# Kernel optimization log

Measured on AMD Instinct MI355X. Metric: run time of the kernel, lower is better.

## Reference

```python
import jax, jax.numpy as jnp
import numpy as np


def _squash(t):
    # squash along axis=2 (the atoms axis of [B, D, A, 1, 1])
    norm = jnp.linalg.norm(t, axis=2, keepdims=True)
    n2 = norm * norm
    return t / norm * (n2 / (1.0 + n2))


def setup_inputs() -> dict:
    key = jax.random.key(0)
    k1, k2 = jax.random.split(key)
    B, I, Ain, D, A = 32, 2048, 16, 32, 16
    x = jax.random.normal(k1, (B, I, Ain, 1, 1), jnp.float32)
    weights = 0.1 * jax.random.normal(k2, (I, Ain, D * A, 1, 1), jnp.float32)
    bias = jnp.full((D, A, 1, 1), 0.1, jnp.float32)  # nn.init.constant_(0.1)
    return {"x": x, "weights": weights, "bias": bias, "num_routing": 3}


def reference(x, weights, bias, num_routing):
    B, I, Ain = x.shape[:3]
    D, A = bias.shape[:2]
    # Vote computation (standard voting): sum over input_atoms.
    # Torch does expand+mul+sum; einsum is the same math without the 4.8GB intermediate.
    votes = jnp.einsum('bia,iao->bio', x[:, :, :, 0, 0],
                       weights[:, :, :, 0, 0]).reshape(B, I, D, A, 1, 1)
    votes_sg = jax.lax.stop_gradient(votes)  # votes_trans_stopped in torch
    logits = jnp.zeros((B, I, D, 1, 1), x.dtype)
    activation = None
    for i in range(num_routing):
        route = jax.nn.softmax(logits, axis=2)  # [B, I, D, 1, 1], softmax over D
        v = votes if i == num_routing - 1 else votes_sg
        # route broadcast over atoms axis; sum over input capsules I
        preact = jnp.sum(route[:, :, :, None] * v, axis=1) + bias  # [B, D, A, 1, 1]
        activation = _squash(preact)
        if i < num_routing - 1:
            # agreement update uses non-stopped votes (as in torch)
            logits = logits + jnp.sum(votes * activation[:, None], axis=3)  # [B, I, D, 1, 1]
    return activation
```

## Files before the change

### kernel.cpp

```cpp
#include <hip/hip_runtime.h>


#define B_  32
#define I_  2048
#define K_  16
#define O_  512
#define NG_ 512
#define IC_ 4

typedef const __attribute__((address_space(1))) uint32_t* gp_t;
typedef __attribute__((address_space(3))) uint32_t* lp_t;

template<int PASS>
__global__ __launch_bounds__(512, 4)
void sweep_kernel(const float* __restrict__ x, const float* __restrict__ W,
                  const float* __restrict__ act0_g, const float* __restrict__ act1_g,
                  float* __restrict__ partial)
{
    const int tid  = threadIdx.x;
    const int lane = tid & 63;
    const int wave = tid >> 6;
    const int ig   = blockIdx.x;
    const int obase = lane * 8;

    const int wv    = __builtin_amdgcn_readfirstlane(wave);
    const int bbase = wv * 4;

    __shared__ float sW[K_ * O_];

    float facc[4][8];
    #pragma unroll
    for (int bb = 0; bb < 4; ++bb)
        #pragma unroll
        for (int j = 0; j < 8; ++j) facc[bb][j] = 0.f;

    float as[4][8];
    if (PASS >= 1) {
        #pragma unroll
        for (int bb = 0; bb < 4; ++bb) {
            const float4* p0 = (const float4*)(act0_g + (bbase + bb) * O_ + obase);
            float4 f0 = p0[0], f1 = p0[1];
            as[bb][0]=f0.x; as[bb][1]=f0.y; as[bb][2]=f0.z; as[bb][3]=f0.w;
            as[bb][4]=f1.x; as[bb][5]=f1.y; as[bb][6]=f1.z; as[bb][7]=f1.w;
            if (PASS == 2) {
                const float4* p1 = (const float4*)(act1_g + (bbase + bb) * O_ + obase);
                float4 g0 = p1[0], g1 = p1[1];
                as[bb][0]+=g0.x; as[bb][1]+=g0.y; as[bb][2]+=g0.z; as[bb][3]+=g0.w;
                as[bb][4]+=g1.x; as[bb][5]+=g1.y; as[bb][6]+=g1.z; as[bb][7]+=g1.w;
            }
        }
    }

    for (int ii = 0; ii < IC_; ++ii) {
        const int i = ig * IC_ + ii;
        __syncthreads();
        {
            const float* gsrc = W + (size_t)i * (K_ * O_);
            #pragma unroll
            for (int q = 0; q < 4; ++q) {
                const int fb = (wave * 4 + q) * 64;
                __builtin_amdgcn_global_load_lds(
                    (gp_t)(gsrc + 4 * (fb + lane)),
                    (lp_t)(&sW[4 * fb]), 16, 0, 0);
            }
        }
        float xs[4][16];
        #pragma unroll
        for (int bb = 0; bb < 4; ++bb) {
            const float4* xp = (const float4*)(x + ((size_t)(bbase + bb) * I_ + i) * K_);
            #pragma unroll
            for (int q = 0; q < 4; ++q) {
                float4 v = xp[q];
                xs[bb][4*q+0]=v.x; xs[bb][4*q+1]=v.y; xs[bb][4*q+2]=v.z; xs[bb][4*q+3]=v.w;
            }
        }
        __syncthreads();

        float V[4][8];
        #pragma unroll
        for (int bb = 0; bb < 4; ++bb)
            #pragma unroll
            for (int j = 0; j < 8; ++j) V[bb][j] = 0.f;
        #pragma unroll
        for (int k = 0; k < K_; ++k) {
            const float4 w0 = *(const float4*)&sW[k * O_ + obase];
            const float4 w1 = *(const float4*)&sW[k * O_ + obase + 4];
            const float w[8] = {w0.x, w0.y, w0.z, w0.w, w1.x, w1.y, w1.z, w1.w};
            #pragma unroll
            for (int bb = 0; bb < 4; ++bb) {
                const float xb = xs[bb][k];
                #pragma unroll
                for (int j = 0; j < 8; ++j) V[bb][j] = fmaf(xb, w[j], V[bb][j]);
            }
        }

        #pragma unroll
        for (int bb = 0; bb < 4; ++bb) {
            if (PASS == 0) {
                #pragma unroll
                for (int j = 0; j < 8; ++j) facc[bb][j] += V[bb][j];
            } else {
                float lg = 0.f;
                #pragma unroll
                for (int j = 0; j < 8; ++j) lg = fmaf(V[bb][j], as[bb][j], lg);
                lg += __shfl_xor(lg, 1);
                const float e = __expf(lg);
                float s = e;
                s += __shfl_xor(s, 2);
                s += __shfl_xor(s, 4);
                s += __shfl_xor(s, 8);
                s += __shfl_xor(s, 16);
                s += __shfl_xor(s, 32);
                const float r = e * __builtin_amdgcn_rcpf(s);
                #pragma unroll
                for (int j = 0; j < 8; ++j)
                    facc[bb][j] = fmaf(r, V[bb][j], facc[bb][j]);
            }
        }
    }

    #pragma unroll
    for (int bb = 0; bb < 4; ++bb) {
        const int b = bbase + bb;
        float4* dst = (float4*)(partial + ((size_t)ig * B_ + b) * O_ + obase);
        dst[0] = make_float4(facc[bb][0], facc[bb][1], facc[bb][2], facc[bb][3]);
        dst[1] = make_float4(facc[bb][4], facc[bb][5], facc[bb][6], facc[bb][7]);
    }
}

__global__ __launch_bounds__(256)
void reduce_squash(const float* __restrict__ partial, const float* __restrict__ bias,
                   float scale, float* __restrict__ out)
{
    const int t     = threadIdx.x;
    const int quad  = t & 15;
    const int slice = t >> 4;
    const int gbase = blockIdx.x * 64;
    const float4* src = (const float4*)partial + (gbase >> 2) + quad;

    float4 acc = make_float4(0.f, 0.f, 0.f, 0.f);
    #pragma unroll 8
    for (int w = slice * 32; w < slice * 32 + 32; ++w) {
        float4 v = src[(size_t)w * (B_ * O_ / 4)];
        acc.x += v.x; acc.y += v.y; acc.z += v.z; acc.w += v.w;
    }
    __shared__ float4 red[256];
    red[t] = acc;
    __syncthreads();
    if (t < 64) {
        float s = 0.f;
        #pragma unroll
        for (int sl = 0; sl < 16; ++sl)
            s += ((const float*)&red[sl * 16 + (t >> 2)])[t & 3];
        const float p = fmaf(s, scale, bias[(gbase + t) & (O_ - 1)]);
        float nn = p * p;
        nn += __shfl_xor(nn, 1);
        nn += __shfl_xor(nn, 2);
        nn += __shfl_xor(nn, 4);
        nn += __shfl_xor(nn, 8);
        out[gbase + t] = p * sqrtf(nn) / (1.f + nn);
    }
}

extern "C" void kernel_launch(void* const* d_in, const int* in_sizes, int n_in,
                              void* d_out, int out_size, void* d_ws, size_t ws_size,
                              hipStream_t stream) {
    const float* x    = (const float*)d_in[0];
    const float* W    = (const float*)d_in[1];
    const float* bias = (const float*)d_in[2];
    float* out = (float*)d_out;

    float* partial = (float*)d_ws;
    float* act0    = partial + (size_t)NG_ * B_ * O_;
    float* act1    = act0 + B_ * O_;

    sweep_kernel<0><<<NG_, 512, 0, stream>>>(x, W, nullptr, nullptr, partial);
    reduce_squash<<<256, 256, 0, stream>>>(partial, bias, 1.f / 32.f, act0);
    sweep_kernel<1><<<NG_, 512, 0, stream>>>(x, W, act0, nullptr, partial);
    reduce_squash<<<256, 256, 0, stream>>>(partial, bias, 1.f, act1);
    sweep_kernel<2><<<NG_, 512, 0, stream>>>(x, W, act0, act1, partial);
    reduce_squash<<<256, 256, 0, stream>>>(partial, bias, 1.f, out);
}
```

Before: 218.2 us.

## Split batch across blocks, double-buffer two capsules, fold activation sum into reduce

Measured after the change: 233.1 us. 6.8% more time.

```diff
diff --git a/kernel.cpp b/kernel.cpp
--- a/kernel.cpp
+++ b/kernel.cpp
@@ -5,28 +5,28 @@
 #define I_  2048
 #define K_  16
 #define O_  512
-#define NG_ 512
-#define IC_ 4
+#define NG_ 256
+#define IC_ 8
 
 typedef const __attribute__((address_space(1))) uint32_t* gp_t;
 typedef __attribute__((address_space(3))) uint32_t* lp_t;
 
-template<int PASS>
-__global__ __launch_bounds__(512, 4)
+template<bool ROUTED>
+__global__ __launch_bounds__(256)
 void sweep_kernel(const float* __restrict__ x, const float* __restrict__ W,
-                  const float* __restrict__ act0_g, const float* __restrict__ act1_g,
-                  float* __restrict__ partial)
+                  const float* __restrict__ act, float* __restrict__ partial)
 {
     const int tid  = threadIdx.x;
     const int lane = tid & 63;
     const int wave = tid >> 6;
-    const int ig   = blockIdx.x;
-    const int obase = lane * 8;
-
+    const int ig   = blockIdx.x >> 1;
+    const int bh   = blockIdx.x & 1;
     const int wv    = __builtin_amdgcn_readfirstlane(wave);
-    const int bbase = wv * 4;
-
-    __shared__ float sW[K_ * O_];
+    const int bbase = bh * 16 + wv * 4;
+    const int ob1  = lane * 4;
+    const int ob2  = 256 + lane * 4;
+
+    __shared__ float sW[2 * K_ * O_];
 
     float facc[4][8];
     #pragma unroll
@@ -35,86 +35,104 @@
         for (int j = 0; j < 8; ++j) facc[bb][j] = 0.f;
 
     float as[4][8];
-    if (PASS >= 1) {
+    if (ROUTED) {
         #pragma unroll
         for (int bb = 0; bb < 4; ++bb) {
-            const float4* p0 = (const float4*)(act0_g + (bbase + bb) * O_ + obase);
-            float4 f0 = p0[0], f1 = p0[1];
+            const float4 f0 = *(const float4*)(act + (bbase + bb) * O_ + ob1);
+            const float4 f1 = *(const float4*)(act + (bbase + bb) * O_ + ob2);
             as[bb][0]=f0.x; as[bb][1]=f0.y; as[bb][2]=f0.z; as[bb][3]=f0.w;
             as[bb][4]=f1.x; as[bb][5]=f1.y; as[bb][6]=f1.z; as[bb][7]=f1.w;
-            if (PASS == 2) {
-                const float4* p1 = (const float4*)(act1_g + (bbase + bb) * O_ + obase);
-                float4 g0 = p1[0], g1 = p1[1];
-                as[bb][0]+=g0.x; as[bb][1]+=g0.y; as[bb][2]+=g0.z; as[bb][3]+=g0.w;
-                as[bb][4]+=g1.x; as[bb][5]+=g1.y; as[bb][6]+=g1.z; as[bb][7]+=g1.w;
-            }
         }
     }
 
-    for (int ii = 0; ii < IC_; ++ii) {
-        const int i = ig * IC_ + ii;
+    for (int r = 0; r < IC_ / 2; ++r) {
+        const int i0 = ig * IC_ + 2 * r;
         __syncthreads();
         {
-            const float* gsrc = W + (size_t)i * (K_ * O_);
-            #pragma unroll
-            for (int q = 0; q < 4; ++q) {
-                const int fb = (wave * 4 + q) * 64;
+            const float* g0 = W + (size_t)i0 * (K_ * O_);
+            #pragma unroll
+            for (int q = 0; q < 8; ++q) {
+                const int c = wave * 8 + q;
                 __builtin_amdgcn_global_load_lds(
-                    (gp_t)(gsrc + 4 * (fb + lane)),
-                    (lp_t)(&sW[4 * fb]), 16, 0, 0);
-            }
-        }
-        float xs[4][16];
-        #pragma unroll
-        for (int bb = 0; bb < 4; ++bb) {
-            const float4* xp = (const float4*)(x + ((size_t)(bbase + bb) * I_ + i) * K_);
-            #pragma unroll
-            for (int q = 0; q < 4; ++q) {
-                float4 v = xp[q];
-                xs[bb][4*q+0]=v.x; xs[bb][4*q+1]=v.y; xs[bb][4*q+2]=v.z; xs[bb][4*q+3]=v.w;
+                    (gp_t)(g0 + c * 256 + lane * 4),
+                    (lp_t)(sW + c * 256), 16, 0, 0);
+                __builtin_amdgcn_global_load_lds(
+                    (gp_t)(g0 + K_ * O_ + c * 256 + lane * 4),
+                    (lp_t)(sW + K_ * O_ + c * 256), 16, 0, 0);
             }
         }
         __syncthreads();
 
-        float V[4][8];
-        #pragma unroll
-        for (int bb = 0; bb < 4; ++bb)
-            #pragma unroll
-            for (int j = 0; j < 8; ++j) V[bb][j] = 0.f;
-        #pragma unroll
-        for (int k = 0; k < K_; ++k) {
-            const float4 w0 = *(const float4*)&sW[k * O_ + obase];
-            const float4 w1 = *(const float4*)&sW[k * O_ + obase + 4];
-            const float w[8] = {w0.x, w0.y, w0.z, w0.w, w1.x, w1.y, w1.z, w1.w};
+        #pragma unroll
+        for (int half = 0; half < 2; ++half) {
+            const int i = i0 + half;
+            const float* buf = sW + half * (K_ * O_);
+
+            float xs[4][16];
             #pragma unroll
             for (int bb = 0; bb < 4; ++bb) {
-                const float xb = xs[bb][k];
+                const float4* xp =
+                    (const float4*)(x + ((size_t)(bbase + bb) * I_ + i) * K_);
                 #pragma unroll
-                for (int j = 0; j < 8; ++j) V[bb][j] = fmaf(xb, w[j], V[bb][j]);
-            }
-        }
-
-        #pragma unroll
-        for (int bb = 0; bb < 4; ++bb) {
-            if (PASS == 0) {
+                for (int q = 0; q < 4; ++q) {
+                    float4 v = xp[q];
+                    xs[bb][4*q+0]=v.x; xs[bb][4*q+1]=v.y;
+                    xs[bb][4*q+2]=v.z; xs[bb][4*q+3]=v.w;
+                }
+            }
+
+            float V[4][8];
+            #pragma unroll
+            for (int bb = 0; bb < 4; ++bb)
                 #pragma unroll
-                for (int j = 0; j < 8; ++j) facc[bb][j] += V[bb][j];
-            } else {
-                float lg = 0.f;
+                for (int j = 0; j < 8; ++j) V[bb][j] = 0.f;
+            #pragma unroll
+            for (int k = 0; k < K_; ++k) {
+                const float4 w0 = *(const float4*)&buf[k * O_ + ob1];
+                const float4 w1 = *(const float4*)&buf[k * O_ + ob2];
                 #pragma unroll
-                for (int j = 0; j < 8; ++j) lg = fmaf(V[bb][j], as[bb][j], lg);
-                lg += __shfl_xor(lg, 1);
-                const float e = __expf(lg);
-                float s = e;
-                s += __shfl_xor(s, 2);
-                s += __shfl_xor(s, 4);
-                s += __shfl_xor(s, 8);
-                s += __shfl_xor(s, 16);
-                s += __shfl_xor(s, 32);
-                const float r = e * __builtin_amdgcn_rcpf(s);
-                #pragma unroll
-                for (int j = 0; j < 8; ++j)
-                    facc[bb][j] = fmaf(r, V[bb][j], facc[bb][j]);
+                for (int bb = 0; bb < 4; ++bb) {
+                    const float xb = xs[bb][k];
+                    V[bb][0] = fmaf(xb, w0.x, V[bb][0]);
+                    V[bb][1] = fmaf(xb, w0.y, V[bb][1]);
+                    V[bb][2] = fmaf(xb, w0.z, V[bb][2]);
+                    V[bb][3] = fmaf(xb, w0.w, V[bb][3]);
+                    V[bb][4] = fmaf(xb, w1.x, V[bb][4]);
+                    V[bb][5] = fmaf(xb, w1.y, V[bb][5]);
+                    V[bb][6] = fmaf(xb, w1.z, V[bb][6]);
+                    V[bb][7] = fmaf(xb, w1.w, V[bb][7]);
+                }
+            }
+
+            #pragma unroll
+            for (int bb = 0; bb < 4; ++bb) {
+                if (!ROUTED) {
+                    #pragma unroll
+                    for (int j = 0; j < 8; ++j) facc[bb][j] += V[bb][j];
+                } else {
+                    float p1 = 0.f, p2 = 0.f;
+                    #pragma unroll
+                    for (int j = 0; j < 4; ++j) {
+                        p1 = fmaf(V[bb][j],     as[bb][j],     p1);
+                        p2 = fmaf(V[bb][j + 4], as[bb][j + 4], p2);
+                    }
+                    p1 += __shfl_xor(p1, 1);  p1 += __shfl_xor(p1, 2);
+                    p2 += __shfl_xor(p2, 1);  p2 += __shfl_xor(p2, 2);
+                    const float e1 = __expf(p1);
+                    const float e2 = __expf(p2);
+                    float s = e1 + e2;
+                    s += __shfl_xor(s, 4);
+                    s += __shfl_xor(s, 8);
+                    s += __shfl_xor(s, 16);
+                    s += __shfl_xor(s, 32);
+                    const float inv = __builtin_amdgcn_rcpf(s);
+                    const float r1 = e1 * inv, r2 = e2 * inv;
+                    #pragma unroll
+                    for (int j = 0; j < 4; ++j) {
+                        facc[bb][j]     = fmaf(r1, V[bb][j],     facc[bb][j]);
+                        facc[bb][j + 4] = fmaf(r2, V[bb][j + 4], facc[bb][j + 4]);
+                    }
+                }
             }
         }
     }
@@ -122,43 +140,47 @@
     #pragma unroll
     for (int bb = 0; bb < 4; ++bb) {
         const int b = bbase + bb;
-        float4* dst = (float4*)(partial + ((size_t)ig * B_ + b) * O_ + obase);
-        dst[0] = make_float4(facc[bb][0], facc[bb][1], facc[bb][2], facc[bb][3]);
-        dst[1] = make_float4(facc[bb][4], facc[bb][5], facc[bb][6], facc[bb][7]);
+        *(float4*)&partial[((size_t)ig * B_ + b) * O_ + ob1] =
+            make_float4(facc[bb][0], facc[bb][1], facc[bb][2], facc[bb][3]);
+        *(float4*)&partial[((size_t)ig * B_ + b) * O_ + ob2] =
+            make_float4(facc[bb][4], facc[bb][5], facc[bb][6], facc[bb][7]);
     }
 }
 
 __global__ __launch_bounds__(256)
 void reduce_squash(const float* __restrict__ partial, const float* __restrict__ bias,
-                   float scale, float* __restrict__ out)
+                   float scale, const float* __restrict__ addbase,
+                   float* __restrict__ dst)
 {
     const int t     = threadIdx.x;
-    const int quad  = t & 15;
-    const int slice = t >> 4;
-    const int gbase = blockIdx.x * 64;
-    const float4* src = (const float4*)partial + (gbase >> 2) + quad;
+    const int gbase = blockIdx.x * 32;
+    const int q     = t & 7;
+    const int sl    = t >> 3;
+    const float4* src = (const float4*)partial + (gbase >> 2) + q;
 
     float4 acc = make_float4(0.f, 0.f, 0.f, 0.f);
-    #pragma unroll 8
-    for (int w = slice * 32; w < slice * 32 + 32; ++w) {
-        float4 v = src[(size_t)w * (B_ * O_ / 4)];
+    #pragma unroll
+    for (int r = 0; r < 8; ++r) {
+        float4 v = src[(size_t)(sl * 8 + r) * (B_ * O_ / 4)];
         acc.x += v.x; acc.y += v.y; acc.z += v.z; acc.w += v.w;
     }
     __shared__ float4 red[256];
     red[t] = acc;
     __syncthreads();
-    if (t < 64) {
-        float s = 0.f;
-        #pragma unroll
-        for (int sl = 0; sl < 16; ++sl)
-            s += ((const float*)&red[sl * 16 + (t >> 2)])[t & 3];
-        const float p = fmaf(s, scale, bias[(gbase + t) & (O_ - 1)]);
+    if (t < 32) {
+        float v = 0.f;
+        #pragma unroll
+        for (int s = 0; s < 32; ++s)
+            v += ((const float*)&red[s * 8 + (t >> 2)])[t & 3];
+        const float p = fmaf(v, scale, bias[(gbase + t) & (O_ - 1)]);
         float nn = p * p;
         nn += __shfl_xor(nn, 1);
         nn += __shfl_xor(nn, 2);
         nn += __shfl_xor(nn, 4);
         nn += __shfl_xor(nn, 8);
-        out[gbase + t] = p * sqrtf(nn) / (1.f + nn);
+        float o = p * sqrtf(nn) / (1.f + nn);
+        if (addbase) o += addbase[gbase + t];
+        dst[gbase + t] = o;
     }
 }
 
@@ -172,12 +194,12 @@
 
     float* partial = (float*)d_ws;
     float* act0    = partial + (size_t)NG_ * B_ * O_;
-    float* act1    = act0 + B_ * O_;
-
-    sweep_kernel<0><<<NG_, 512, 0, stream>>>(x, W, nullptr, nullptr, partial);
-    reduce_squash<<<256, 256, 0, stream>>>(partial, bias, 1.f / 32.f, act0);
-    sweep_kernel<1><<<NG_, 512, 0, stream>>>(x, W, act0, nullptr, partial);
-    reduce_squash<<<256, 256, 0, stream>>>(partial, bias, 1.f, act1);
-    sweep_kernel<2><<<NG_, 512, 0, stream>>>(x, W, act0, act1, partial);
-    reduce_squash<<<256, 256, 0, stream>>>(partial, bias, 1.f, out);
+    float* asum    = act0 + B_ * O_;
+
+    sweep_kernel<false><<<NG_ * 2, 256, 0, stream>>>(x, W, nullptr, partial);
+    reduce_squash<<<512, 256, 0, stream>>>(partial, bias, 1.f / 32.f, nullptr, act0);
+    sweep_kernel<true><<<NG_ * 2, 256, 0, stream>>>(x, W, act0, partial);
+    reduce_squash<<<512, 256, 0, stream>>>(partial, bias, 1.f, act0, asum);
+    sweep_kernel<true><<<NG_ * 2, 256, 0, stream>>>(x, W, asum, partial);
+    reduce_squash<<<512, 256, 0, stream>>>(partial, bias, 1.f, nullptr, out);
 }
```
